# Kernel tuning notes

Measured on AMD Instinct MI355X. Metric: run time of the kernel, lower is better.

Reference implementation:

```python
import jax, jax.numpy as jnp
import numpy as np

D_MODEL = 1024
N_HEADS = 16
D_HEAD = D_MODEL // N_HEADS
D_FF = 4096
BATCH = 2
SEQ = 2048
LN_EPS = 1e-5


def setup_inputs() -> dict:
    key = jax.random.key(0)
    ks = jax.random.split(key, 12)
    s = 1.0 / np.sqrt(D_MODEL)
    x = jax.random.normal(ks[0], (BATCH, SEQ, D_MODEL), dtype=jnp.float32)
    mask = jnp.broadcast_to(jnp.tril(jnp.ones((SEQ, SEQ), jnp.int32)), (BATCH, SEQ, SEQ))
    return {
        "x": x,
        "mask": mask,
        # per-head projections stacked: [H, D, Dh] (bias=False in source)
        "Wq": jax.random.normal(ks[1], (N_HEADS, D_MODEL, D_HEAD), jnp.float32) * s,
        "Wk": jax.random.normal(ks[2], (N_HEADS, D_MODEL, D_HEAD), jnp.float32) * s,
        "Wv": jax.random.normal(ks[3], (N_HEADS, D_MODEL, D_HEAD), jnp.float32) * s,
        "Wo": jax.random.normal(ks[4], (D_MODEL, D_MODEL), jnp.float32) * s,
        "ln1_w": jnp.ones((D_MODEL,), jnp.float32),
        "ln1_b": jnp.zeros((D_MODEL,), jnp.float32),
        "ln2_w": jnp.ones((D_MODEL,), jnp.float32),
        "ln2_b": jnp.zeros((D_MODEL,), jnp.float32),
        "W1": jax.random.normal(ks[5], (D_MODEL, D_FF), jnp.float32) * s,
        "b1": jnp.zeros((D_FF,), jnp.float32),
        "W2": jax.random.normal(ks[6], (D_FF, D_MODEL), jnp.float32) * (1.0 / np.sqrt(D_FF)),
        "b2": jnp.zeros((D_MODEL,), jnp.float32),
    }


def layer_norm(x, w, b):
    mu = jnp.mean(x, axis=-1, keepdims=True)
    var = jnp.var(x, axis=-1, keepdims=True)
    return (x - mu) * jax.lax.rsqrt(var + LN_EPS) * w + b


def reference(x, mask, Wq, Wk, Wv, Wo, ln1_w, ln1_b, ln2_w, ln2_b, W1, b1, W2, b2):
    # pre-LN masked self-attention
    h = layer_norm(x, ln1_w, ln1_b)
    q = jnp.einsum("bsd,hde->bhse", h, Wq)  # [B,H,S,Dh]
    k = jnp.einsum("bsd,hde->bhse", h, Wk)
    v = jnp.einsum("bsd,hde->bhse", h, Wv)
    scores = jnp.einsum("bhse,bhte->bhst", q, k) / np.sqrt(D_HEAD)
    scores = jnp.where(mask[:, None, :, :].astype(bool), scores, -jnp.inf)
    weights = jax.nn.softmax(scores, axis=-1)
    attn = jnp.einsum("bhst,bhte->bhse", weights, v)  # [B,H,S,Dh]
    # concat heads (head order = last-dim order in torch.cat)
    concat = attn.transpose(0, 2, 1, 3).reshape(x.shape[0], x.shape[1], D_MODEL)
    att_out = concat @ Wo
    att_x = x + att_out
    # FFN with exact (erf) GELU, matching nn.GELU default
    h2 = layer_norm(att_x, ln2_w, ln2_b)
    ff = jax.nn.gelu(h2 @ W1 + b1, approximate=False) @ W2 + b2
    return att_x + ff
```

## Files before the change

### kernel.cpp

```cpp
#include <hip/hip_runtime.h>
#include <hip/hip_bf16.h>
#include <math.h>

#define D_MODEL 1024
#define N_HEADS 16
#define D_HEAD  64
#define D_FF    4096
#define BATCH   2
#define SEQ     2048
#define NTOK    (BATCH*SEQ)

typedef __hip_bfloat16 bf16;
typedef __attribute__((ext_vector_type(8))) short short8;
typedef __attribute__((ext_vector_type(4))) float floatx4;

template<typename TIN>
__global__ void ln_kernel(const TIN* __restrict__ x,
                          const float* __restrict__ w,
                          const float* __restrict__ b,
                          bf16* __restrict__ out) {
    int row = blockIdx.x;
    int tid = threadIdx.x;
    const long base = (long)row * D_MODEL;
    float v[4];
    float s = 0.f, sq = 0.f;
#pragma unroll
    for (int i = 0; i < 4; ++i) {
        float xv = (float)x[base + tid + i*256];
        v[i] = xv; s += xv; sq += xv*xv;
    }
    __shared__ float r1[256], r2[256];
    r1[tid] = s; r2[tid] = sq; __syncthreads();
    for (int off = 128; off > 0; off >>= 1) {
        if (tid < off) { r1[tid] += r1[tid+off]; r2[tid] += r2[tid+off]; }
        __syncthreads();
    }
    float mean = r1[0] * (1.f/D_MODEL);
    float var  = r2[0] * (1.f/D_MODEL) - mean*mean;
    float rstd = rsqrtf(var + 1e-5f);
#pragma unroll
    for (int i = 0; i < 4; ++i) {
        int c = tid + i*256;
        out[base + c] = __float2bfloat16((v[i] - mean) * rstd * w[c] + b[c]);
    }
}

__global__ __launch_bounds__(256) void wcvt_kernel(const float* __restrict__ W,
                                                   bf16* __restrict__ Wt,
                                                   int K, int N) {
    __shared__ float t[32][33];
    int n0 = blockIdx.x * 32, k0 = blockIdx.y * 32;
    int lx = threadIdx.x & 31, ly = threadIdx.x >> 5;
#pragma unroll
    for (int i = 0; i < 4; ++i) {
        int k = ly + i * 8;
        t[k][lx] = W[(long)(k0 + k) * N + n0 + lx];
    }
    __syncthreads();
#pragma unroll
    for (int i = 0; i < 4; ++i) {
        int n = ly + i * 8;
        Wt[(long)(n0 + n) * K + k0 + lx] = __float2bfloat16(t[lx][n]);
    }
}

__global__ __launch_bounds__(256) void wcvt_wo_w1(const float* __restrict__ Wo,
                                                  const float* __restrict__ W1,
                                                  bf16* __restrict__ wo_bf,
                                                  bf16* __restrict__ w1_bf) {
    __shared__ float t[32][33];
    int gx = blockIdx.x;
    const float* W; bf16* Wt; int N, n0;
    if (gx < 32) { W = Wo; Wt = wo_bf; N = D_MODEL; n0 = gx * 32; }
    else         { W = W1; Wt = w1_bf; N = D_FF;    n0 = (gx - 32) * 32; }
    int k0 = blockIdx.y * 32;
    int lx = threadIdx.x & 31, ly = threadIdx.x >> 5;
#pragma unroll
    for (int i = 0; i < 4; ++i) {
        int k = ly + i * 8;
        t[k][lx] = W[(long)(k0 + k) * N + n0 + lx];
    }
    __syncthreads();
#pragma unroll
    for (int i = 0; i < 4; ++i) {
        int n = ly + i * 8;
        Wt[(long)(n0 + n) * D_MODEL + k0 + lx] = __float2bfloat16(t[lx][n]);
    }
}

__global__ __launch_bounds__(256) void wcvt_qkv(const float* __restrict__ Wq,
                                                const float* __restrict__ Wk,
                                                const float* __restrict__ Wv,
                                                bf16* __restrict__ outp) {
    __shared__ float t[32][33];
    int z = blockIdx.z, mat = z >> 4, head = z & 15;
    const float* W = (mat == 0 ? Wq : mat == 1 ? Wk : Wv) + (long)head * D_MODEL * D_HEAD;
    bf16* Wt = outp + (long)z * D_HEAD * D_MODEL;
    int n0 = blockIdx.x * 32, k0 = blockIdx.y * 32;
    int lx = threadIdx.x & 31, ly = threadIdx.x >> 5;
#pragma unroll
    for (int i = 0; i < 4; ++i) {
        int k = ly + i * 8;
        t[k][lx] = W[(long)(k0 + k) * D_HEAD + n0 + lx];
    }
    __syncthreads();
#pragma unroll
    for (int i = 0; i < 4; ++i) {
        int n = ly + i * 8;
        Wt[(long)(n0 + n) * D_MODEL + k0 + lx] = __float2bfloat16(t[lx][n]);
    }
}

__device__ inline void swz2d(int& bx, int& by) {
    int gx = gridDim.x;
    int nwg = gx * gridDim.y;
    int bid = blockIdx.y * gx + blockIdx.x;
    int swz = (bid & 7) * (nwg >> 3) + (bid >> 3);
    bx = swz % gx;
    by = swz / gx;
}

template<int ROWS>
__device__ inline void stage_tile(const bf16* g, int gstride, short* lds) {
    int lane = threadIdx.x & 63, wave = threadIdx.x >> 6;
#pragma unroll
    for (int it = 0; it < ROWS / 64; ++it) {
        int c = wave + it * 4;
        const bf16* gp = g + (long)(c * 16 + (lane >> 2)) * gstride + (lane & 3) * 8;
        short* lp = lds + c * 512 + lane * 8;
        __builtin_amdgcn_global_load_lds(
            (const __attribute__((address_space(1))) void*)gp,
            (__attribute__((address_space(3))) void*)lp, 16, 0, 0);
    }
}

#define G256_BAR  asm volatile("s_barrier" ::: "memory")
#define G256_VM12 asm volatile("s_waitcnt vmcnt(12)" ::: "memory")
#define G256_VM6  asm volatile("s_waitcnt vmcnt(6)" ::: "memory")
#define G256_VM4  asm volatile("s_waitcnt vmcnt(4)" ::: "memory")
#define G256_VM0  asm volatile("s_waitcnt vmcnt(0)" ::: "memory")
#define G256_LGKM0 do { asm volatile("s_waitcnt lgkmcnt(0)" ::: "memory"); \
                        __builtin_amdgcn_sched_barrier(0); } while (0)

__device__ inline short8 rd128(unsigned ad) {
    short8 r;
    asm volatile("ds_read_b128 %0, %1" : "=v"(r) : "v"(ad));
    return r;
}

template<int BM, int BN, int BK, int BIAS, int ACT, int RES, int OUTBF16>
__global__ __launch_bounds__(256) void mfma_gemm_pipe3(
    const bf16* __restrict__ A, int lda,
    const bf16* __restrict__ Wt, int K,
    const float* __restrict__ bias, const float* __restrict__ resid,
    void* __restrict__ Cout, int ldc)
{
    constexpr int MI  = BM / 32;
    constexpr int NR  = BN / 32;
    constexpr int ASZ = BM * BK;
    constexpr int BSZ = BN * BK;
    __shared__ short As[3 * BM * BK];
    __shared__ short Bs[3 * BN * BK];
    int bx, by; swz2d(bx, by);
    int row0 = by * BM, col0 = bx * BN;
    int tid = threadIdx.x, wave = tid >> 6, lane = tid & 63;
    int quad = lane >> 4, l16 = lane & 15;
    int wm = (wave >> 1) * (BM / 2);
    int wn = (wave & 1) * (BN / 2);
    const int NT = K / BK;

    auto stage = [&](int t, int buf) {
        int k0 = t * BK;
#pragma unroll
        for (int kk = 0; kk < BK; kk += 32) {
            stage_tile<BM>(A  + (long)row0 * lda + k0 + kk, lda,
                           As + buf * ASZ + (kk / 32) * BM * 32);
            stage_tile<BN>(Wt + (long)col0 * K   + k0 + kk, K,
                           Bs + buf * BSZ + (kk / 32) * BN * 32);
        }
    };

    unsigned asbase = (unsigned)(unsigned long long)(void*)&As[0];
    unsigned bsbase = (unsigned)(unsigned long long)(void*)&Bs[0];
    unsigned aRow[MI], bRow[NR];
#pragma unroll
    for (int mi = 0; mi < MI; ++mi)
        aRow[mi] = (unsigned)(((wm + mi * 16 + l16) * 32 + quad * 8) * 2);
#pragma unroll
    for (int ni = 0; ni < NR; ++ni)
        bRow[ni] = (unsigned)(((wn + ni * 16 + l16) * 32 + quad * 8) * 2);

    floatx4 acc[MI][NR];
#pragma unroll
    for (int mi = 0; mi < MI; ++mi)
#pragma unroll
        for (int ni = 0; ni < NR; ++ni)
            acc[mi][ni] = (floatx4){0.f, 0.f, 0.f, 0.f};

    stage(0, 0);
    if (NT > 1) stage(1, 1);
    if (NT > 2) stage(2, 2);

    int buf = 0;
    for (int i = 0; i < NT; ++i) {
        if (i + 2 < NT)      { G256_VM12; }
        else if (i + 1 < NT) { G256_VM6;  }
        else                 { G256_VM0;  }
        G256_BAR;

        short8 af[BK / 32][MI], bfr[BK / 32][NR];
#pragma unroll
        for (int p = 0; p < BK / 32; ++p) {
            unsigned ab = asbase + (unsigned)((buf * ASZ + p * BM * 32) * 2);
            unsigned bb = bsbase + (unsigned)((buf * BSZ + p * BN * 32) * 2);
#pragma unroll
            for (int mi = 0; mi < MI; ++mi) af[p][mi] = rd128(ab + aRow[mi]);
#pragma unroll
            for (int ni = 0; ni < NR; ++ni) bfr[p][ni] = rd128(bb + bRow[ni]);
        }
        G256_LGKM0;
#pragma unroll
        for (int p = 0; p < BK / 32; ++p)
#pragma unroll
            for (int mi = 0; mi < MI; ++mi)
#pragma unroll
                for (int ni = 0; ni < NR; ++ni)
                    acc[mi][ni] = __builtin_amdgcn_mfma_f32_16x16x32_bf16(
                        af[p][mi], bfr[p][ni], acc[mi][ni], 0, 0, 0);

        G256_BAR;
        if (i + 3 < NT) stage(i + 3, buf);
        buf = (buf == 2) ? 0 : buf + 1;
    }

#pragma unroll
    for (int mi = 0; mi < MI; ++mi) {
#pragma unroll
        for (int ni = 0; ni < NR; ++ni) {
#pragma unroll
            for (int r = 0; r < 4; ++r) {
                int row = row0 + wm + mi * 16 + quad * 4 + r;
                int col = col0 + wn + ni * 16 + l16;
                float v = acc[mi][ni][r];
                if (BIAS) v += bias[col];
                if (ACT == 1) {
                    float x2 = v * v;
                    float arg = fminf(v * fmaf(0.1029392f, x2, 2.3021182f), 20.f);
                    float t = exp2f(arg);
                    v = v * t * __builtin_amdgcn_rcpf(t + 1.f);
                }
                long idx = (long)row * ldc + col;
                if (RES == 1) v += resid[idx];
                if (OUTBF16) ((bf16*)Cout)[idx] = __float2bfloat16(v);
                else         ((float*)Cout)[idx] = v;
            }
        }
    }
}

struct QkvOut { bf16* o[3]; };

#define RG(buf,mat,kh) (((buf)*4 + (mat)*2 + (kh)) * 8192)

__device__ inline void stage2(const bf16* g0, const bf16* g1, int koff, short* lp) {
    __builtin_amdgcn_global_load_lds(
        (const __attribute__((address_space(1))) void*)(g0 + koff),
        (__attribute__((address_space(3))) void*)lp, 16, 0, 0);
    __builtin_amdgcn_global_load_lds(
        (const __attribute__((address_space(1))) void*)(g1 + koff),
        (__attribute__((address_space(3))) void*)(lp + 4096), 16, 0, 0);
}

template<int MH>
__device__ inline void rd_frags_asm(unsigned ldsbase, int ra, int rb,
                                    const unsigned (&aoff)[8], const unsigned (&boff)[4],
                                    short8 (&areg)[4], short8 (&breg)[4]) {
    if (MH == 0) {
#pragma unroll
        for (int ni = 0; ni < 4; ++ni) {
            unsigned ad = ldsbase + (unsigned)(rb * 2) + boff[ni];
            asm volatile("ds_read_b128 %0, %1" : "=v"(breg[ni]) : "v"(ad));
        }
    }
#pragma unroll
    for (int mi = 0; mi < 4; ++mi) {
        unsigned ad = ldsbase + (unsigned)(ra * 2) + aoff[MH * 4 + mi];
        asm volatile("ds_read_b128 %0, %1" : "=v"(areg[mi]) : "v"(ad));
    }
}

template<int MH>
__device__ inline void do_mfma16(const short8 (&areg)[4], const short8 (&breg)[4],
                                 floatx4 (&acc)[8][4]) {
    __builtin_amdgcn_s_setprio(1);
#pragma unroll
    for (int mi = 0; mi < 4; ++mi)
#pragma unroll
        for (int ni = 0; ni < 4; ++ni)
            acc[MH * 4 + mi][ni] = __builtin_amdgcn_mfma_f32_16x16x32_bf16(
                areg[mi], breg[ni], acc[MH * 4 + mi][ni], 0, 0, 0);
    __builtin_amdgcn_s_setprio(0);
}

template<int EPI>
__global__ __launch_bounds__(512, 1) void gemm256_kernel(
    const bf16* __restrict__ A, int lda,
    const bf16* __restrict__ Wt, int ldw, int K,
    const float* __restrict__ bias,
    bf16* __restrict__ Cout, int ldc, QkvOut qa)
{
    __shared__ short lds[65536];
    const int NT = K / 64;
    int bx, by; swz2d(bx, by);
    int row0 = by * 256, col0 = bx * 256;
    int tid = threadIdx.x;
    int lane = tid & 63, wave = tid >> 6;
    int quad = lane >> 4, l16 = lane & 15;
    int wr = wave >> 2, wc = wave & 3;

    int srow = tid >> 2, slot = tid & 3;
    int cA0 = slot ^ ((srow >> 1) & 3);
    int cA1 = slot ^ (((srow + 128) >> 1) & 3);
    const bf16* a0 = A  + (long)(row0 + srow) * lda + cA0 * 8;
    const bf16* a1 = A  + (long)(row0 + srow + 128) * lda + cA1 * 8;
    const bf16* b0 = Wt + (long)(col0 + srow) * ldw + cA0 * 8;
    const bf16* b1 = Wt + (long)(col0 + srow + 128) * ldw + cA1 * 8;
    short* lt = lds + tid * 8;

    unsigned ldsbase = (unsigned)(unsigned long long)(void*)&lds[0];
    unsigned aoff[8], boff[4];
#pragma unroll
    for (int mi = 0; mi < 8; ++mi) {
        int row = wr * 128 + mi * 16 + l16;
        int sl = quad ^ ((row >> 1) & 3);
        aoff[mi] = (unsigned)((row * 32 + sl * 8) * 2);
    }
#pragma unroll
    for (int ni = 0; ni < 4; ++ni) {
        int row = wc * 64 + ni * 16 + l16;
        int sl = quad ^ ((row >> 1) & 3);
        boff[ni] = (unsigned)((row * 32 + sl * 8) * 2);
    }

    floatx4 acc[8][4];
#pragma unroll
    for (int mi = 0; mi < 8; ++mi)
#pragma unroll
        for (int ni = 0; ni < 4; ++ni)
            acc[mi][ni] = (floatx4){0.f, 0.f, 0.f, 0.f};

    stage2(a0, a1, 0,  lt + RG(0,0,0));
    stage2(b0, b1, 0,  lt + RG(0,1,0));
    stage2(a0, a1, 32, lt + RG(0,0,1));
    stage2(b0, b1, 32, lt + RG(0,1,1));
    stage2(a0, a1, 64, lt + RG(1,0,0));
    stage2(b0, b1, 64, lt + RG(1,1,0));
    G256_VM4;
    G256_BAR;

    short8 areg[4], breg[4];

    for (int i = 0; i < NT / 2; ++i) {
        int T = 2 * i;
        bool s2 = (T + 2 < NT);
        bool s3 = (T + 3 < NT);
        int k1off = (T + 1) * 64;
        int k2off = (T + 2) * 64;
        int k3off = (T + 3) * 64;

        rd_frags_asm<0>(ldsbase, RG(0,0,0), RG(0,1,0), aoff, boff, areg, breg);
        stage2(a0, a1, k1off + 32, lt + RG(1,0,1));
        G256_BAR;
        G256_LGKM0;
        do_mfma16<0>(areg, breg, acc);
        G256_BAR;

        rd_frags_asm<1>(ldsbase, RG(0,0,0), RG(0,1,0), aoff, boff, areg, breg);
        stage2(b0, b1, k1off + 32, lt + RG(1,1,1));
        G256_BAR;
        G256_LGKM0;
        do_mfma16<1>(areg, breg, acc);
        G256_BAR;

        rd_frags_asm<0>(ldsbase, RG(0,0,1), RG(0,1,1), aoff, boff, areg, breg);
        if (s2) stage2(a0, a1, k2off, lt + RG(0,0,0));
        G256_BAR;
        G256_LGKM0;
        do_mfma16<0>(areg, breg, acc);
        G256_BAR;

        rd_frags_asm<1>(ldsbase, RG(0,0,1), RG(0,1,1), aoff, boff, areg, breg);
        if (s2) stage2(b0, b1, k2off, lt + RG(0,1,0));
        G256_BAR;
        G256_LGKM0;
        do_mfma16<1>(areg, breg, acc);
        if (s2) { G256_VM4; } else { G256_VM0; }
        G256_BAR;

        rd_frags_asm<0>(ldsbase, RG(1,0,0), RG(1,1,0), aoff, boff, areg, breg);
        if (s2) stage2(a0, a1, k2off + 32, lt + RG(0,0,1));
        G256_BAR;
        G256_LGKM0;
        do_mfma16<0>(areg, breg, acc);
        G256_BAR;

        rd_frags_asm<1>(ldsbase, RG(1,0,0), RG(1,1,0), aoff, boff, areg, breg);
        if (s2) stage2(b0, b1, k2off + 32, lt + RG(0,1,1));
        G256_BAR;
        G256_LGKM0;
        do_mfma16<1>(areg, breg, acc);
        G256_BAR;

        rd_frags_asm<0>(ldsbase, RG(1,0,1), RG(1,1,1), aoff, boff, areg, breg);
        if (s3) stage2(a0, a1, k3off, lt + RG(1,0,0));
        G256_BAR;
        G256_LGKM0;
        do_mfma16<0>(areg, breg, acc);
        G256_BAR;

        rd_frags_asm<1>(ldsbase, RG(1,0,1), RG(1,1,1), aoff, boff, areg, breg);
        if (s3) stage2(b0, b1, k3off, lt + RG(1,1,0));
        G256_BAR;
        G256_LGKM0;
        do_mfma16<1>(areg, breg, acc);
        if (s3) { G256_VM4; } else { G256_VM0; }
        G256_BAR;
    }

#pragma unroll
    for (int mi = 0; mi < 8; ++mi) {
#pragma unroll
        for (int ni = 0; ni < 4; ++ni) {
#pragma unroll
            for (int r = 0; r < 4; ++r) {
                int row = row0 + wr * 128 + mi * 16 + quad * 4 + r;
                int col = col0 + wc * 64 + ni * 16 + l16;
                float v = acc[mi][ni][r];
                if constexpr (EPI == 0) {
                    v += bias[col];
                    float x2 = v * v;
                    float arg = fminf(v * fmaf(0.1029392f, x2, 2.3021182f), 20.f);
                    float t = exp2f(arg);
                    v = v * t * __builtin_amdgcn_rcpf(t + 1.f);
                    Cout[(long)row * ldc + col] = __float2bfloat16(v);
                } else {
                    int mat = col >> 10, hd = (col >> 6) & 15, d = col & 63;
                    int b = row >> 11, s = row & 2047;
                    qa.o[mat][(((long)(b * 16 + hd) * SEQ + s) << 6) + d] =
                        __float2bfloat16(v);
                }
            }
        }
    }
}

__global__ __launch_bounds__(256) void fattn_mfma(const bf16* __restrict__ q,
                                                  const bf16* __restrict__ k,
                                                  const bf16* __restrict__ v,
                                                  bf16* __restrict__ po,
                                                  float* __restrict__ lz) {
    int byr = blockIdx.y;
    int tile = (byr < 8) ? byr : 23 - byr;
    int chunk = blockIdx.z;
    int bh = blockIdx.x;
    int tid = threadIdx.x;
    int wave = tid >> 6, lane = tid & 63;
    int quad = lane >> 4, l16 = lane & 15;
    const long base = (long)bh * SEQ * D_HEAD;
    const int r0g = tile * 128;

    bf16*  pob = po + (long)chunk * 32 * SEQ * 64;
    float* lzb = lz + (long)chunk * 32 * SEQ;

    __shared__ short Ks[64 * 72];
    __shared__ short Vt[64 * 72];
    __shared__ short Ps[4][32 * 72];

    short8 qf[2][2];
#pragma unroll
    for (int rb = 0; rb < 2; ++rb) {
        const short* qrow = (const short*)(q + base +
            (long)(r0g + wave * 32 + rb * 16 + l16) * D_HEAD);
        qf[rb][0] = *(const short8*)(qrow + quad * 8);
        qf[rb][1] = *(const short8*)(qrow + 32 + quad * 8);
#pragma unroll
        for (int c = 0; c < 2; ++c)
#pragma unroll
            for (int j = 0; j < 8; ++j) {
                float f = __uint_as_float(((unsigned)(unsigned short)qf[rb][c][j]) << 16)
                          * 0.18033688f;
                qf[rb][c][j] = __builtin_bit_cast(short, __float2bfloat16(f));
            }
    }

    short8 onesf;
    {
        short o1 = (l16 == 0) ? (short)0x3F80 : (short)0;
#pragma unroll
        for (int j = 0; j < 8; ++j) onesf[j] = o1;
    }

    floatx4 o[2][4];
#pragma unroll
    for (int rb = 0; rb < 2; ++rb)
#pragma unroll
        for (int nb = 0; nb < 4; ++nb) o[rb][nb] = (floatx4){0.f, 0.f, 0.f, 0.f};
    floatx4 l4[2] = {(floatx4){0.f,0.f,0.f,0.f}, (floatx4){0.f,0.f,0.f,0.f}};

    const int kt0 = chunk ? tile + 1 : 0;
    const int kt1 = chunk ? 2 * tile + 1 : tile;

    uint4 kr0, kr1, va4, vb4;
    auto ldKV = [&](int kt) {
        const short* krow = (const short*)(k + base +
            (long)(kt * 64 + (tid >> 2)) * D_HEAD);
        int c = tid & 3;
        kr0 = *(const uint4*)(krow + c * 16);
        kr1 = *(const uint4*)(krow + c * 16 + 8);
        int tp = (tid & 31) * 2;
        int d0 = ((tid >> 5) & 7) * 8;
        const short* v0 = (const short*)(v + base + (long)(kt * 64 + tp) * D_HEAD + d0);
        va4 = *(const uint4*)v0;
        vb4 = *(const uint4*)(v0 + D_HEAD);
    };

    ldKV(kt0);

    for (int kt = kt0; kt <= kt1; ++kt) {
        __syncthreads();
        {
            int t = tid >> 2, c = tid & 3;
            *(uint4*)&Ks[t * 72 + c * 16]     = kr0;
            *(uint4*)&Ks[t * 72 + c * 16 + 8] = kr1;
        }
        {
            int tp = (tid & 31) * 2;
            int d0 = ((tid >> 5) & 7) * 8;
            short va[8], vb[8];
            *(uint4*)va = va4;
            *(uint4*)vb = vb4;
#pragma unroll
            for (int j = 0; j < 8; ++j) {
                unsigned pk = (unsigned)(unsigned short)va[j] |
                              ((unsigned)(unsigned short)vb[j] << 16);
                *(unsigned*)&Vt[(d0 + j) * 72 + tp] = pk;
            }
        }
        if (kt < kt1) ldKV(kt + 1);
        __syncthreads();

        if (kt * 64 > r0g + wave * 32 + 31) continue;

        floatx4 s[2][4];
        __builtin_amdgcn_s_setprio(1);
#pragma unroll
        for (int nb = 0; nb < 4; ++nb) {
            short8 kf0 = *(const short8*)&Ks[(nb * 16 + l16) * 72 + quad * 8];
            short8 kf1 = *(const short8*)&Ks[(nb * 16 + l16) * 72 + 32 + quad * 8];
#pragma unroll
            for (int rb = 0; rb < 2; ++rb) {
                floatx4 z4 = (floatx4){0.f, 0.f, 0.f, 0.f};
                z4 = __builtin_amdgcn_mfma_f32_16x16x32_bf16(qf[rb][0], kf0, z4, 0, 0, 0);
                z4 = __builtin_amdgcn_mfma_f32_16x16x32_bf16(qf[rb][1], kf1, z4, 0, 0, 0);
                s[rb][nb] = z4;
            }
        }
        __builtin_amdgcn_s_setprio(0);

        if (kt >= 2 * tile) {
#pragma unroll
            for (int rb = 0; rb < 2; ++rb) {
                int qg = r0g + wave * 32 + rb * 16 + quad * 4;
#pragma unroll
                for (int nb = 0; nb < 4; ++nb) {
                    int kg = kt * 64 + nb * 16 + l16;
#pragma unroll
                    for (int r = 0; r < 4; ++r)
                        if (kg > qg + r) s[rb][nb][r] = -1e30f;
                }
            }
        }

        short* Pw = &Ps[wave][0];
#pragma unroll
        for (int rb = 0; rb < 2; ++rb)
#pragma unroll
            for (int nb = 0; nb < 4; ++nb)
#pragma unroll
                for (int r = 0; r < 4; ++r) {
                    float p = exp2f(s[rb][nb][r]);
                    Pw[(rb * 16 + quad * 4 + r) * 72 + nb * 16 + l16] =
                        __builtin_bit_cast(short, __float2bfloat16(p));
                }

        short8 pf[2][2];
#pragma unroll
        for (int rb = 0; rb < 2; ++rb) {
            pf[rb][0] = *(const short8*)&Pw[(rb * 16 + l16) * 72 + quad * 8];
            pf[rb][1] = *(const short8*)&Pw[(rb * 16 + l16) * 72 + 32 + quad * 8];
        }
        __builtin_amdgcn_s_setprio(1);
#pragma unroll
        for (int nb = 0; nb < 4; ++nb) {
            short8 vf0 = *(const short8*)&Vt[(nb * 16 + l16) * 72 + quad * 8];
            short8 vf1 = *(const short8*)&Vt[(nb * 16 + l16) * 72 + 32 + quad * 8];
#pragma unroll
            for (int rb = 0; rb < 2; ++rb) {
                o[rb][nb] = __builtin_amdgcn_mfma_f32_16x16x32_bf16(pf[rb][0], vf0, o[rb][nb], 0, 0, 0);
                o[rb][nb] = __builtin_amdgcn_mfma_f32_16x16x32_bf16(pf[rb][1], vf1, o[rb][nb], 0, 0, 0);
            }
        }
#pragma unroll
        for (int rb = 0; rb < 2; ++rb) {
            l4[rb] = __builtin_amdgcn_mfma_f32_16x16x32_bf16(pf[rb][0], onesf, l4[rb], 0, 0, 0);
            l4[rb] = __builtin_amdgcn_mfma_f32_16x16x32_bf16(pf[rb][1], onesf, l4[rb], 0, 0, 0);
        }
        __builtin_amdgcn_s_setprio(0);
    }

#pragma unroll
    for (int rb = 0; rb < 2; ++rb) {
#pragma unroll
        for (int nb = 0; nb < 4; ++nb)
#pragma unroll
            for (int r = 0; r < 4; ++r) {
                int row = r0g + wave * 32 + rb * 16 + quad * 4 + r;
                pob[((long)bh * SEQ + row) * 64 + nb * 16 + l16] =
                    __float2bfloat16(o[rb][nb][r]);
            }
        if (l16 == 0) {
#pragma unroll
            for (int r = 0; r < 4; ++r) {
                int row = r0g + wave * 32 + rb * 16 + quad * 4 + r;
                lzb[(long)bh * SEQ + row] = l4[rb][r];
            }
        }
    }
}

__global__ __launch_bounds__(256) void attn_combine(const bf16* __restrict__ po,
                                                    const float* __restrict__ lz,
                                                    bf16* __restrict__ cc) {
    const long CH = 32L * SEQ * 64;
    int row = blockIdx.x;
    int b = row >> 11, s = row & 2047;
    int tid = threadIdx.x;
    int col = tid * 4;
    int h = col >> 6, d = col & 63;
    long pidx = ((long)(b * 16 + h) * SEQ + s) * 64 + d;
    uint2 u0 = *(const uint2*)((const unsigned short*)po + pidx);
    uint2 u1 = *(const uint2*)((const unsigned short*)po + CH + pidx);
    long li = (long)(b * 16 + h) * SEQ + s;
    float linv = 1.f / (lz[li] + lz[32L * SEQ + li]);
    unsigned ua[4] = {u0.x & 0xFFFFu, u0.x >> 16, u0.y & 0xFFFFu, u0.y >> 16};
    unsigned ub[4] = {u1.x & 0xFFFFu, u1.x >> 16, u1.y & 0xFFFFu, u1.y >> 16};
    unsigned short rr[4];
#pragma unroll
    for (int i = 0; i < 4; ++i) {
        float ov = __uint_as_float(ua[i] << 16) + __uint_as_float(ub[i] << 16);
        rr[i] = __builtin_bit_cast(unsigned short, __float2bfloat16(ov * linv));
    }
    uint2 w;
    w.x = (unsigned)rr[0] | ((unsigned)rr[1] << 16);
    w.y = (unsigned)rr[2] | ((unsigned)rr[3] << 16);
    *(uint2*)((unsigned short*)cc + (long)row * D_MODEL + col) = w;
}

extern "C" void kernel_launch(void* const* d_in, const int* in_sizes, int n_in,
                              void* d_out, int out_size, void* d_ws, size_t ws_size,
                              hipStream_t stream) {
    const float* x    = (const float*)d_in[0];
    const float* Wq   = (const float*)d_in[2];
    const float* Wk   = (const float*)d_in[3];
    const float* Wv   = (const float*)d_in[4];
    const float* Wo   = (const float*)d_in[5];
    const float* ln1w = (const float*)d_in[6];
    const float* ln1b = (const float*)d_in[7];
    const float* ln2w = (const float*)d_in[8];
    const float* ln2b = (const float*)d_in[9];
    const float* W1   = (const float*)d_in[10];
    const float* b1   = (const float*)d_in[11];
    const float* W2   = (const float*)d_in[12];
    const float* b2   = (const float*)d_in[13];
    float* out = (float*)d_out;

    char* wsb = (char*)d_ws;
    const size_t MB = 1024*1024;
    bf16*  h1      = (bf16*)(wsb + 0*MB);
    bf16*  qb      = (bf16*)(wsb + 8*MB);
    bf16*  kb      = (bf16*)(wsb + 16*MB);
    bf16*  vb      = (bf16*)(wsb + 24*MB);
    bf16*  wqkv_bf = (bf16*)(wsb + 32*MB);
    bf16*  po      = (bf16*)(wsb + 32*MB);
    float* lz      = (float*)(wsb + 48*MB);
    bf16*  cc      = (bf16*)(wsb + 0*MB);
    bf16*  wo_bf   = (bf16*)(wsb + 8*MB);
    bf16*  w1_bf   = (bf16*)(wsb + 10*MB);
    bf16*  h2      = (bf16*)(wsb + 0*MB);
    bf16*  ff      = (bf16*)(wsb + 24*MB);
    bf16*  w2_bf   = (bf16*)(wsb + 8*MB);

    QkvOut qa; qa.o[0] = qb; qa.o[1] = kb; qa.o[2] = vb;
    QkvOut qdummy = {};

    ln_kernel<float><<<NTOK, 256, 0, stream>>>(x, ln1w, ln1b, h1);

    wcvt_qkv<<<dim3(2, 32, 48), 256, 0, stream>>>(Wq, Wk, Wv, wqkv_bf);

    gemm256_kernel<1><<<dim3(12, 16), 512, 0, stream>>>(
        h1, D_MODEL, wqkv_bf, D_MODEL, D_MODEL, nullptr, nullptr, 0, qa);

    fattn_mfma<<<dim3(BATCH*N_HEADS, SEQ/128, 2), 256, 0, stream>>>(qb, kb, vb, po, lz);

    attn_combine<<<NTOK, 256, 0, stream>>>(po, lz, cc);

    wcvt_wo_w1<<<dim3(160, 32), 256, 0, stream>>>(Wo, W1, wo_bf, w1_bf);

    mfma_gemm_pipe3<64,128,64,0,0,1,0><<<dim3(8,64), 256, 0, stream>>>(
        cc, D_MODEL, wo_bf, D_MODEL, nullptr, x, out, D_MODEL);

    ln_kernel<float><<<NTOK, 256, 0, stream>>>(out, ln2w, ln2b, h2);

    gemm256_kernel<0><<<dim3(16, 16), 512, 0, stream>>>(
        h2, D_MODEL, w1_bf, D_MODEL, D_MODEL, b1, ff, D_FF, qdummy);

    wcvt_kernel<<<dim3(D_MODEL/32, D_FF/32), 256, 0, stream>>>(W2, w2_bf, D_FF, D_MODEL);

    mfma_gemm_pipe3<64,128,64,1,0,1,0><<<dim3(8,64), 256, 0, stream>>>(
        ff, D_FF, w2_bf, D_FF, b2, out, out, D_MODEL);
}
```

Before: 358.8 us.

## Double flash-attention query tile to 256 rows per block with 64 rows per wave

```diff
diff --git a/kernel.cpp b/kernel.cpp
--- a/kernel.cpp
+++ b/kernel.cpp
@@ -460,14 +460,14 @@
                                                   bf16* __restrict__ po,
                                                   float* __restrict__ lz) {
     int byr = blockIdx.y;
-    int tile = (byr < 8) ? byr : 23 - byr;
     int chunk = blockIdx.z;
+    int tile = chunk ? 7 - byr : byr;
     int bh = blockIdx.x;
     int tid = threadIdx.x;
     int wave = tid >> 6, lane = tid & 63;
     int quad = lane >> 4, l16 = lane & 15;
     const long base = (long)bh * SEQ * D_HEAD;
-    const int r0g = tile * 128;
+    const int r0g = tile * 256;
 
     bf16*  pob = po + (long)chunk * 32 * SEQ * 64;
     float* lzb = lz + (long)chunk * 32 * SEQ;
@@ -476,11 +476,11 @@
     __shared__ short Vt[64 * 72];
     __shared__ short Ps[4][32 * 72];
 
-    short8 qf[2][2];
-#pragma unroll
-    for (int rb = 0; rb < 2; ++rb) {
+    short8 qf[4][2];
+#pragma unroll
+    for (int rb = 0; rb < 4; ++rb) {
         const short* qrow = (const short*)(q + base +
-            (long)(r0g + wave * 32 + rb * 16 + l16) * D_HEAD);
+            (long)(r0g + wave * 64 + rb * 16 + l16) * D_HEAD);
         qf[rb][0] = *(const short8*)(qrow + quad * 8);
         qf[rb][1] = *(const short8*)(qrow + 32 + quad * 8);
 #pragma unroll
@@ -500,15 +500,17 @@
         for (int j = 0; j < 8; ++j) onesf[j] = o1;
     }
 
-    floatx4 o[2][4];
-#pragma unroll
-    for (int rb = 0; rb < 2; ++rb)
+    floatx4 o[4][4];
+#pragma unroll
+    for (int rb = 0; rb < 4; ++rb)
 #pragma unroll
         for (int nb = 0; nb < 4; ++nb) o[rb][nb] = (floatx4){0.f, 0.f, 0.f, 0.f};
-    floatx4 l4[2] = {(floatx4){0.f,0.f,0.f,0.f}, (floatx4){0.f,0.f,0.f,0.f}};
-
-    const int kt0 = chunk ? tile + 1 : 0;
-    const int kt1 = chunk ? 2 * tile + 1 : tile;
+    floatx4 l4[4];
+#pragma unroll
+    for (int rb = 0; rb < 4; ++rb) l4[rb] = (floatx4){0.f, 0.f, 0.f, 0.f};
+
+    const int kt0 = chunk ? 2 * tile + 2 : 0;
+    const int kt1 = chunk ? 4 * tile + 3 : 2 * tile + 1;
 
     uint4 kr0, kr1, va4, vb4;
     auto ldKV = [&](int kt) {
@@ -549,89 +551,97 @@
         if (kt < kt1) ldKV(kt + 1);
         __syncthreads();
 
-        if (kt * 64 > r0g + wave * 32 + 31) continue;
-
-        floatx4 s[2][4];
-        __builtin_amdgcn_s_setprio(1);
-#pragma unroll
-        for (int nb = 0; nb < 4; ++nb) {
-            short8 kf0 = *(const short8*)&Ks[(nb * 16 + l16) * 72 + quad * 8];
-            short8 kf1 = *(const short8*)&Ks[(nb * 16 + l16) * 72 + 32 + quad * 8];
-#pragma unroll
-            for (int rb = 0; rb < 2; ++rb) {
-                floatx4 z4 = (floatx4){0.f, 0.f, 0.f, 0.f};
-                z4 = __builtin_amdgcn_mfma_f32_16x16x32_bf16(qf[rb][0], kf0, z4, 0, 0, 0);
-                z4 = __builtin_amdgcn_mfma_f32_16x16x32_bf16(qf[rb][1], kf1, z4, 0, 0, 0);
-                s[rb][nb] = z4;
-            }
-        }
-        __builtin_amdgcn_s_setprio(0);
-
-        if (kt >= 2 * tile) {
-#pragma unroll
-            for (int rb = 0; rb < 2; ++rb) {
-                int qg = r0g + wave * 32 + rb * 16 + quad * 4;
-#pragma unroll
-                for (int nb = 0; nb < 4; ++nb) {
-                    int kg = kt * 64 + nb * 16 + l16;
-#pragma unroll
-                    for (int r = 0; r < 4; ++r)
-                        if (kg > qg + r) s[rb][nb][r] = -1e30f;
+        if (kt * 64 > r0g + wave * 64 + 63) continue;
+        bool domask = (kt >= 4 * tile + wave);
+
+        short* Pw = &Ps[wave][0];
+#pragma unroll
+        for (int h = 0; h < 2; ++h) {
+            floatx4 s[2][4];
+            __builtin_amdgcn_s_setprio(1);
+#pragma unroll
+            for (int nb = 0; nb < 4; ++nb) {
+                short8 kf0 = *(const short8*)&Ks[(nb * 16 + l16) * 72 + quad * 8];
+                short8 kf1 = *(const short8*)&Ks[(nb * 16 + l16) * 72 + 32 + quad * 8];
+#pragma unroll
+                for (int rr = 0; rr < 2; ++rr) {
+                    floatx4 z4 = (floatx4){0.f, 0.f, 0.f, 0.f};
+                    z4 = __builtin_amdgcn_mfma_f32_16x16x32_bf16(qf[2*h+rr][0], kf0, z4, 0, 0, 0);
+                    z4 = __builtin_amdgcn_mfma_f32_16x16x32_bf16(qf[2*h+rr][1], kf1, z4, 0, 0, 0);
+                    s[rr][nb] = z4;
                 }
             }
-        }
-
-        short* Pw = &Ps[wave][0];
-#pragma unroll
-        for (int rb = 0; rb < 2; ++rb)
-#pragma unroll
-            for (int nb = 0; nb < 4; ++nb)
-#pragma unroll
-                for (int r = 0; r < 4; ++r) {
-                    float p = exp2f(s[rb][nb][r]);
-                    Pw[(rb * 16 + quad * 4 + r) * 72 + nb * 16 + l16] =
-                        __builtin_bit_cast(short, __float2bfloat16(p));
+            __builtin_amdgcn_s_setprio(0);
+
+            if (domask) {
+#pragma unroll
+                for (int rr = 0; rr < 2; ++rr) {
+                    int qg = r0g + wave * 64 + (2*h+rr) * 16 + quad * 4;
+#pragma unroll
+                    for (int nb = 0; nb < 4; ++nb) {
+                        int kg = kt * 64 + nb * 16 + l16;
+#pragma unroll
+                        for (int r = 0; r < 4; ++r)
+                            if (kg > qg + r) s[rr][nb][r] = -1e30f;
+                    }
                 }
-
-        short8 pf[2][2];
-#pragma unroll
-        for (int rb = 0; rb < 2; ++rb) {
-            pf[rb][0] = *(const short8*)&Pw[(rb * 16 + l16) * 72 + quad * 8];
-            pf[rb][1] = *(const short8*)&Pw[(rb * 16 + l16) * 72 + 32 + quad * 8];
-        }
-        __builtin_amdgcn_s_setprio(1);
-#pragma unroll
-        for (int nb = 0; nb < 4; ++nb) {
-            short8 vf0 = *(const short8*)&Vt[(nb * 16 + l16) * 72 + quad * 8];
-            short8 vf1 = *(const short8*)&Vt[(nb * 16 + l16) * 72 + 32 + quad * 8];
-#pragma unroll
-            for (int rb = 0; rb < 2; ++rb) {
-                o[rb][nb] = __builtin_amdgcn_mfma_f32_16x16x32_bf16(pf[rb][0], vf0, o[rb][nb], 0, 0, 0);
-                o[rb][nb] = __builtin_amdgcn_mfma_f32_16x16x32_bf16(pf[rb][1], vf1, o[rb][nb], 0, 0, 0);
-            }
-        }
-#pragma unroll
-        for (int rb = 0; rb < 2; ++rb) {
-            l4[rb] = __builtin_amdgcn_mfma_f32_16x16x32_bf16(pf[rb][0], onesf, l4[rb], 0, 0, 0);
-            l4[rb] = __builtin_amdgcn_mfma_f32_16x16x32_bf16(pf[rb][1], onesf, l4[rb], 0, 0, 0);
-        }
-        __builtin_amdgcn_s_setprio(0);
-    }
-
-#pragma unroll
-    for (int rb = 0; rb < 2; ++rb) {
+            }
+
+#pragma unroll
+            for (int rr = 0; rr < 2; ++rr)
+#pragma unroll
+                for (int nb = 0; nb < 4; ++nb)
+#pragma unroll
+                    for (int r = 0; r < 4; ++r) {
+                        float p = exp2f(s[rr][nb][r]);
+                        Pw[(rr * 16 + quad * 4 + r) * 72 + nb * 16 + l16] =
+                            __builtin_bit_cast(short, __float2bfloat16(p));
+                    }
+
+            short8 pf[2][2];
+#pragma unroll
+            for (int rr = 0; rr < 2; ++rr) {
+                pf[rr][0] = *(const short8*)&Pw[(rr * 16 + l16) * 72 + quad * 8];
+                pf[rr][1] = *(const short8*)&Pw[(rr * 16 + l16) * 72 + 32 + quad * 8];
+            }
+            __builtin_amdgcn_s_setprio(1);
+#pragma unroll
+            for (int nb = 0; nb < 4; ++nb) {
+                short8 vf0 = *(const short8*)&Vt[(nb * 16 + l16) * 72 + quad * 8];
+                short8 vf1 = *(const short8*)&Vt[(nb * 16 + l16) * 72 + 32 + quad * 8];
+#pragma unroll
+                for (int rr = 0; rr < 2; ++rr) {
+                    o[2*h+rr][nb] = __builtin_amdgcn_mfma_f32_16x16x32_bf16(
+                        pf[rr][0], vf0, o[2*h+rr][nb], 0, 0, 0);
+                    o[2*h+rr][nb] = __builtin_amdgcn_mfma_f32_16x16x32_bf16(
+                        pf[rr][1], vf1, o[2*h+rr][nb], 0, 0, 0);
+                }
+            }
+#pragma unroll
+            for (int rr = 0; rr < 2; ++rr) {
+                l4[2*h+rr] = __builtin_amdgcn_mfma_f32_16x16x32_bf16(
+                    pf[rr][0], onesf, l4[2*h+rr], 0, 0, 0);
+                l4[2*h+rr] = __builtin_amdgcn_mfma_f32_16x16x32_bf16(
+                    pf[rr][1], onesf, l4[2*h+rr], 0, 0, 0);
+            }
+            __builtin_amdgcn_s_setprio(0);
+        }
+    }
+
+#pragma unroll
+    for (int rb = 0; rb < 4; ++rb) {
 #pragma unroll
         for (int nb = 0; nb < 4; ++nb)
 #pragma unroll
             for (int r = 0; r < 4; ++r) {
-                int row = r0g + wave * 32 + rb * 16 + quad * 4 + r;
+                int row = r0g + wave * 64 + rb * 16 + quad * 4 + r;
                 pob[((long)bh * SEQ + row) * 64 + nb * 16 + l16] =
                     __float2bfloat16(o[rb][nb][r]);
             }
         if (l16 == 0) {
 #pragma unroll
             for (int r = 0; r < 4; ++r) {
-                int row = r0g + wave * 32 + rb * 16 + quad * 4 + r;
+                int row = r0g + wave * 64 + rb * 16 + quad * 4 + r;
                 lzb[(long)bh * SEQ + row] = l4[rb][r];
             }
         }
@@ -710,7 +720,7 @@
     gemm256_kernel<1><<<dim3(12, 16), 512, 0, stream>>>(
         h1, D_MODEL, wqkv_bf, D_MODEL, D_MODEL, nullptr, nullptr, 0, qa);
 
-    fattn_mfma<<<dim3(BATCH*N_HEADS, SEQ/128, 2), 256, 0, stream>>>(qb, kb, vb, po, lz);
+    fattn_mfma<<<dim3(BATCH*N_HEADS, SEQ/256, 2), 256, 0, stream>>>(qb, kb, vb, po, lz);
 
     attn_combine<<<NTOK, 256, 0, stream>>>(po, lz, cc);
 
```

After: 371.1 us. 1.03x slower.
